# Optimization experiments

Measured on AMD Instinct MI355X. Metric: run time of the kernel, lower is better.

## Reference

```python
import jax, jax.numpy as jnp
import numpy as np


def _conv2d(x, w, pad):
    return jax.lax.conv_general_dilated(
        x, w, (1, 1), [(pad, pad), (pad, pad)],
        dimension_numbers=('NCHW', 'OIHW', 'NCHW'))


def _affine_grid(theta, k):
    # torch F.affine_grid, align_corners=False; output size (k, k)
    base = ((2.0 * jnp.arange(k) + 1.0) / k - 1.0).astype(jnp.float32)
    pts = jnp.stack([
        jnp.broadcast_to(base[None, :], (k, k)),  # x varies along width
        jnp.broadcast_to(base[:, None], (k, k)),  # y varies along height
        jnp.ones((k, k), jnp.float32)], -1)        # [k,k,3]
    return jnp.einsum('ijc,nrc->nijr', pts, theta)  # [N,k,k,2] -> (x,y)


def _grid_sample(img, grid):
    # torch F.grid_sample: bilinear, zeros padding, align_corners=False
    # img [C,H,W], grid [k,k,2] with (x,y) in [-1,1]
    C, H, W = img.shape
    gx = (grid[..., 0] + 1.0) * W * 0.5 - 0.5
    gy = (grid[..., 1] + 1.0) * H * 0.5 - 0.5
    x0 = jnp.floor(gx); y0 = jnp.floor(gy)
    wx = gx - x0; wy = gy - y0
    x0i = x0.astype(jnp.int32); y0i = y0.astype(jnp.int32)

    def gath(yi, xi):
        valid = ((xi >= 0) & (xi < W) & (yi >= 0) & (yi < H)).astype(img.dtype)
        v = img[:, jnp.clip(yi, 0, H - 1), jnp.clip(xi, 0, W - 1)]  # [C,k,k]
        return v * valid[None]

    v00 = gath(y0i, x0i); v01 = gath(y0i, x0i + 1)
    v10 = gath(y0i + 1, x0i); v11 = gath(y0i + 1, x0i + 1)
    return (v00 * ((1 - wx) * (1 - wy))[None] + v01 * (wx * (1 - wy))[None]
            + v10 * ((1 - wx) * wy)[None] + v11 * (wx * wy)[None])


def reference(x, stn0_w, stn0_b, stn1_w, lin_w, lin_b, check):
    B, C, H, W = x.shape
    k = stn1_w.shape[-1]
    h = jax.nn.relu(_conv2d(x, stn0_w, k // 2) + stn0_b[None, :, None, None])
    ident6 = jnp.array([1., 0., 0., 0., 1., 0.], jnp.float32)
    out = _conv2d(h, stn1_w, 0) * (1.0 - check) + ident6[None, :, None, None]
    Ho, Wo = out.shape[2], out.shape[3]
    N = B * Ho * Wo
    # permute(0,3,2,1).view(N,2,3) as in torch
    theta = out.transpose(0, 3, 2, 1).reshape(N, 2, 3)
    grid = _affine_grid(theta, k)  # [N,k,k,2]
    xv = jnp.arange(k // 2, k // 2 + Ho, dtype=jnp.float32)[:, None]  # meshgrid 'ij'
    yv = jnp.arange(k // 2, k // 2 + Wo, dtype=jnp.float32)[None, :]
    half = float(k // 2)
    auxx = ((grid[..., 0] * half).reshape(B, Ho, Wo, k, k)
            + xv[None, :, :, None, None]).reshape(N, k, k) / (H - 1) * 2.0 - 1.0
    auxy = ((grid[..., 1] * half).reshape(B, Ho, Wo, k, k)
            + yv[None, :, :, None, None]).reshape(N, k, k) / (W - 1) * 2.0 - 1.0
    auxgrid = jnp.stack([auxx, auxy], -1).reshape(B, Ho * Wo, k, k, 2)
    # tile(x,0,Ho*Wo) duplicates x[b] for each of its Ho*Wo grids; gather directly
    xs = jax.vmap(lambda img, g: jax.vmap(lambda gg: _grid_sample(img, gg))(g))(x, auxgrid)  # [B,P,C,k,k]
    x_out = xs.reshape(N, -1) @ lin_w.T + lin_b  # [N,O]
    score = x_out.reshape(B, Ho, Wo, -1).transpose(0, 3, 2, 1)  # [B,O,Wo,Ho] as in torch
    ident23 = jnp.array([[1., 0., 0.], [0., 1., 0.]], jnp.float32)
    return score, ident23[None] - theta, out, auxx, auxy


def setup_inputs() -> dict:
    key = jax.random.key(0)
    ks = jax.random.split(key, 6)
    C, O, k = 128, 256, 3
    B, H, W = 8, 56, 56
    x = jax.random.normal(ks[0], (B, C, H, W), jnp.float32)
    stn0_w = jax.random.normal(ks[1], (C, C, k, k), jnp.float32) * (1.0 / np.sqrt(C * k * k))
    stn0_b = jax.random.normal(ks[2], (C,), jnp.float32) * 0.01
    # original zero-inits stn1; use small random so theta is non-trivial
    stn1_w = jax.random.normal(ks[3], (6, C, k, k), jnp.float32) * 0.01
    lin_w = jax.random.normal(ks[4], (O, C * k * k), jnp.float32) * (1.0 / np.sqrt(C * k * k))
    lin_b = jax.random.normal(ks[5], (O,), jnp.float32) * 0.01
    return {'x': x, 'stn0_w': stn0_w, 'stn0_b': stn0_b, 'stn1_w': stn1_w,
            'lin_w': lin_w, 'lin_b': lin_b, 'check': 0}
```

## Files before the change

kernel.cpp:

```cpp
#include <hip/hip_runtime.h>

typedef __attribute__((ext_vector_type(4))) float f32x4;
typedef __attribute__((ext_vector_type(8))) short bf16x8;

#define OPLANE 2916
#define NN 23328
#define KDIM 1152
#define PLANE 3136
#define LDP 72

__device__ __forceinline__ unsigned short f2bf(float f) {
    unsigned u = __builtin_bit_cast(unsigned, f);
    u += 0x7fffu + ((u >> 16) & 1u);
    return (unsigned short)(u >> 16);
}
__device__ __forceinline__ float bf2f(unsigned short h) {
    unsigned u = ((unsigned)h) << 16;
    return __builtin_bit_cast(float, u);
}

__global__ __launch_bounds__(256) void k_prep(const float* __restrict__ w0,
                                              const float* __restrict__ lw,
                                              unsigned short* __restrict__ b1t,
                                              unsigned short* __restrict__ b2t) {
    int idx = blockIdx.x * 256 + threadIdx.x;
    if (idx < 147456) {
        int r = idx / KDIM, k = idx - r * KDIM;
        int ij = k >> 7, ic = k & 127;
        b1t[idx] = f2bf(w0[r * KDIM + ic * 9 + ij]);
    } else {
        int j = idx - 147456;
        int r = j / KDIM, k = j - r * KDIM;
        int ij = k >> 7, ic = k & 127;
        b2t[j] = f2bf(lw[r * KDIM + ic * 9 + ij]);
    }
}

__global__ __launch_bounds__(256) void k_nhwc(const float* __restrict__ x,
                                              unsigned short* __restrict__ xnh) {
    __shared__ unsigned short lds[56 * 132];
    const int y = blockIdx.x, b = blockIdx.y, tid = threadIdx.x;
    for (int i = tid; i < 7168; i += 256) {
        int ic = i / 56, xc = i - ic * 56;
        lds[xc * 132 + ic] = f2bf(x[(b * 128 + ic) * PLANE + y * 56 + xc]);
    }
    __syncthreads();
    for (int i = tid; i < 7168; i += 256) {
        int xc = i >> 7, ic = i & 127;
        xnh[(b * PLANE + y * 56 + xc) * 128 + ic] = lds[xc * 132 + ic];
    }
}

__global__ __launch_bounds__(256) void k_gemm1(const unsigned short* __restrict__ xnh,
                                               const unsigned short* __restrict__ Bt,
                                               const float* __restrict__ bias,
                                               float* __restrict__ C) {
    __shared__ unsigned short As[64 * LDP];
    __shared__ unsigned short Bs[64 * LDP];
    const int tid = threadIdx.x;
    const int lane = tid & 63, wid = tid >> 6;
    const int wr = wid >> 1, wc = wid & 1;
    const int n0 = blockIdx.x * 64;
    const int m0 = blockIdx.y * 64;

    f32x4 acc[2][2];
    #pragma unroll
    for (int mt = 0; mt < 2; mt++)
        #pragma unroll
        for (int nt = 0; nt < 2; nt++) { acc[mt][nt][0]=0.f; acc[mt][nt][1]=0.f; acc[mt][nt][2]=0.f; acc[mt][nt][3]=0.f; }

    const int row = tid >> 2, q = tid & 3;
    const int p = m0 + row;
    const int b = p / PLANE; int rem = p - b * PLANE;
    const int y = rem / 56; const int xc = rem - y * 56;
    unsigned short* asw = &As[row * LDP + q * 16];
    const unsigned short* bg = Bt + (n0 + row) * KDIM + q * 16;
    unsigned short* bsw = &Bs[row * LDP + q * 16];
    const int lm = lane & 15, lq = lane >> 4;

    uint4 a0, a1, bv0, bv1;
    auto issue = [&](int it) {
        const int ij = it >> 1;
        const int di = ij / 3, dj = ij - di * 3;
        const int icb = (it & 1) << 6;
        a0 = make_uint4(0u,0u,0u,0u); a1 = make_uint4(0u,0u,0u,0u);
        bool valid = (y + di >= 1) && (y + di <= 56) && (xc + dj >= 1) && (xc + dj <= 56);
        if (valid) {
            const unsigned short* ap = xnh + (p + (di - 1) * 56 + (dj - 1)) * 128 + icb + q * 16;
            a0 = *(const uint4*)ap;
            a1 = *(const uint4*)(ap + 8);
        }
        bv0 = *(const uint4*)(bg + it * 64);
        bv1 = *(const uint4*)(bg + it * 64 + 8);
    };
    issue(0);

    #pragma unroll
    for (int it = 0; it < 18; it++) {
        __syncthreads();
        *(uint4*)(asw + 0) = a0;  *(uint4*)(asw + 8) = a1;
        *(uint4*)(bsw + 0) = bv0; *(uint4*)(bsw + 8) = bv1;
        __syncthreads();
        if (it < 17) issue(it + 1);
        #pragma unroll
        for (int kk = 0; kk < 64; kk += 32) {
            bf16x8 af[2], bf[2];
            #pragma unroll
            for (int mt = 0; mt < 2; mt++)
                af[mt] = *(const bf16x8*)&As[(wr * 32 + mt * 16 + lm) * LDP + kk + lq * 8];
            #pragma unroll
            for (int nt = 0; nt < 2; nt++)
                bf[nt] = *(const bf16x8*)&Bs[(wc * 32 + nt * 16 + lm) * LDP + kk + lq * 8];
            #pragma unroll
            for (int mt = 0; mt < 2; mt++)
                #pragma unroll
                for (int nt = 0; nt < 2; nt++)
                    acc[mt][nt] = __builtin_amdgcn_mfma_f32_16x16x32_bf16(af[mt], bf[nt], acc[mt][nt], 0, 0, 0);
        }
    }
    #pragma unroll
    for (int mt = 0; mt < 2; mt++) {
        int m = m0 + wr * 32 + mt * 16 + lq * 4;
        #pragma unroll
        for (int nt = 0; nt < 2; nt++) {
            int n = n0 + wc * 32 + nt * 16 + lm;
            float bb = bias[n];
            #pragma unroll
            for (int r = 0; r < 4; r++)
                C[(m + r) * 128 + n] = fmaxf(acc[mt][nt][r] + bb, 0.f);
        }
    }
}

__global__ __launch_bounds__(256) void k_conv2f(const float* __restrict__ h,
                                                const float* __restrict__ w1,
                                                const int* __restrict__ check,
                                                float* __restrict__ o_out,
                                                float* __restrict__ o_th,
                                                float* __restrict__ o_ax,
                                                float* __restrict__ o_ay,
                                                float* __restrict__ sxy) {
    __shared__ float wlds[6912];
    __shared__ float red[16 * 6 * 17];
    __shared__ float vals[96];
    const int tid = threadIdx.x;
    for (int idx = tid; idx < 6912; idx += 256) {
        int r = idx / KDIM, k = idx - r * KDIM;
        int ij = k >> 7, ic = k & 127;
        wlds[idx] = w1[r * KDIM + ic * 9 + ij];
    }
    __syncthreads();
    const int pt = tid >> 4, c = tid & 15;
    const int p = blockIdx.x * 16 + pt;
    int b = p / OPLANE; int rem = p - b * OPLANE; int oh = rem / 54; int ow = rem - oh * 54;
    const float4* h4 = (const float4*)h;
    const float4* w4 = (const float4*)wlds;
    float acc[6] = {0.f, 0.f, 0.f, 0.f, 0.f, 0.f};
    const int base_sp = b * PLANE + oh * 56 + ow;
    #pragma unroll
    for (int i = 0; i < 3; i++) {
        #pragma unroll
        for (int j = 0; j < 3; j++) {
            int sp = base_sp + i * 56 + j;
            float4 h0 = h4[sp * 32 + c * 2];
            float4 h1 = h4[sp * 32 + c * 2 + 1];
            int ij = i * 3 + j;
            #pragma unroll
            for (int r = 0; r < 6; r++) {
                float4 wa = w4[r * 288 + ij * 32 + c * 2];
                float4 wb = w4[r * 288 + ij * 32 + c * 2 + 1];
                acc[r] += h0.x * wa.x + h0.y * wa.y + h0.z * wa.z + h0.w * wa.w
                        + h1.x * wb.x + h1.y * wb.y + h1.z * wb.z + h1.w * wb.w;
            }
        }
    }
    #pragma unroll
    for (int r = 0; r < 6; r++) red[(pt * 6 + r) * 17 + c] = acc[r];
    __syncthreads();
    if (tid < 96) {
        const float* rp = &red[tid * 17];
        float s = 0.f;
        #pragma unroll
        for (int e = 0; e < 16; e++) s += rp[e];
        vals[tid] = s;
    }
    __syncthreads();
    if (tid < 16) {
        int p2 = blockIdx.x * 16 + tid;
        int b2 = p2 / OPLANE; int r2 = p2 - b2 * OPLANE; int oh2 = r2 / 54; int ow2 = r2 - oh2 * 54;
        float val[6];
        float s = 1.0f - (float)check[0];
        const float id6[6] = {1.f, 0.f, 0.f, 0.f, 1.f, 0.f};
        #pragma unroll
        for (int r = 0; r < 6; r++) val[r] = vals[tid * 6 + r] * s + id6[r];
        int n = (b2 * 54 + ow2) * 54 + oh2;
        #pragma unroll
        for (int r = 0; r < 6; r++) {
            o_out[((b2 * 6 + r) * 54 + oh2) * 54 + ow2] = val[r];
            o_th[n * 6 + r] = id6[r] - val[r];
        }
        const float bse[3] = {-2.f / 3.f, 0.f, 2.f / 3.f};
        #pragma unroll
        for (int i = 0; i < 3; i++)
            #pragma unroll
            for (int j = 0; j < 3; j++) {
                float gx = bse[j] * val[0] + bse[i] * val[1] + val[2];
                float gy = bse[j] * val[3] + bse[i] * val[4] + val[5];
                float ax = (gx + 1.f + (float)ow2) * (2.f / 55.f) - 1.f;
                float ay = (gy + 1.f + (float)oh2) * (2.f / 55.f) - 1.f;
                int ij = i * 3 + j;
                o_ax[n * 9 + ij] = ax;
                o_ay[n * 9 + ij] = ay;
                sxy[(n * 9 + ij) * 2 + 0] = (ax + 1.f) * 28.f - 0.5f;
                sxy[(n * 9 + ij) * 2 + 1] = (ay + 1.f) * 28.f - 0.5f;
            }
    }
}

__global__ __launch_bounds__(256) void k_sgemm(const unsigned short* __restrict__ xnh,
                                               const unsigned short* __restrict__ Wt,
                                               const float* __restrict__ bias,
                                               const float* __restrict__ sxy,
                                               float* __restrict__ score) {
    __shared__ unsigned short Ss[64 * LDP];
    __shared__ unsigned short Ws[128 * LDP];
    const int tid = threadIdx.x;
    const int lane = tid & 63, wid = tid >> 6;
    const int wr = wid >> 1, wc = wid & 1;
    const int o0 = blockIdx.x * 128;
    const int s0 = blockIdx.y * 64;

    f32x4 acc[4][2];
    #pragma unroll
    for (int mt = 0; mt < 4; mt++)
        #pragma unroll
        for (int nt = 0; nt < 2; nt++) { acc[mt][nt][0]=0.f; acc[mt][nt][1]=0.f; acc[mt][nt][2]=0.f; acc[mt][nt][3]=0.f; }

    const int row = tid >> 2, q = tid & 3;
    const int mp = min(s0 + row, NN - 1);
    const int b = mp / OPLANE; const int rr = mp - b * OPLANE;
    const int ho = rr / 54, wo = rr - (rr / 54) * 54;
    const int n = (b * 54 + wo) * 54 + ho;
    const int xbase = b * PLANE;
    unsigned short* ssw = &Ss[row * LDP + q * 16];
    const int wrow = tid >> 1, wq = tid & 1;
    const unsigned short* wg = Wt + (o0 + wrow) * KDIM + wq * 32;
    unsigned short* wsw = &Ws[wrow * LDP + wq * 32];
    const int lm = lane & 15, lq = lane >> 4;

    float2 sc[9];
    {
        const float* spp = sxy + n * 18;
        #pragma unroll
        for (int ij = 0; ij < 9; ij++) sc[ij] = *(const float2*)(spp + ij * 2);
    }

    int off0 = 0, off1 = 0, off2 = 0, off3 = 0;
    float wt0 = 0.f, wt1 = 0.f, wt2 = 0.f, wt3 = 0.f;
    auto mkoff = [&](int ij) {
        float sx = sc[ij].x, sy = sc[ij].y;
        float x0f = floorf(sx), y0f = floorf(sy);
        float wx = sx - x0f, wy = sy - y0f;
        int x0 = (int)x0f, y0 = (int)y0f;
        int x1 = x0 + 1, y1 = y0 + 1;
        float vx0 = (x0 >= 0 && x0 < 56) ? 1.f : 0.f;
        float vx1 = (x1 >= 0 && x1 < 56) ? 1.f : 0.f;
        float vy0 = (y0 >= 0 && y0 < 56) ? 1.f : 0.f;
        float vy1 = (y1 >= 0 && y1 < 56) ? 1.f : 0.f;
        int xc0 = min(max(x0, 0), 55), xc1 = min(max(x1, 0), 55);
        int yc0 = min(max(y0, 0), 55), yc1 = min(max(y1, 0), 55);
        off0 = (xbase + yc0 * 56 + xc0) << 7;
        off1 = (xbase + yc0 * 56 + xc1) << 7;
        off2 = (xbase + yc1 * 56 + xc0) << 7;
        off3 = (xbase + yc1 * 56 + xc1) << 7;
        wt0 = vy0 * vx0 * (1.f - wx) * (1.f - wy);
        wt1 = vy0 * vx1 * wx * (1.f - wy);
        wt2 = vy1 * vx0 * (1.f - wx) * wy;
        wt3 = vy1 * vx1 * wx * wy;
    };

    uint4 p0a, p0b, p1a, p1b, p2a, p2b, p3a, p3b;
    uint4 w0v, w1v, w2v, w3v;
    auto issue = [&](int it) {
        const int co = ((it & 1) << 6) + q * 16;
        p0a = *(const uint4*)(xnh + off0 + co);
        p0b = *(const uint4*)(xnh + off0 + co + 8);
        p1a = *(const uint4*)(xnh + off1 + co);
        p1b = *(const uint4*)(xnh + off1 + co + 8);
        p2a = *(const uint4*)(xnh + off2 + co);
        p2b = *(const uint4*)(xnh + off2 + co + 8);
        p3a = *(const uint4*)(xnh + off3 + co);
        p3b = *(const uint4*)(xnh + off3 + co + 8);
        w0v = *(const uint4*)(wg + it * 64);
        w1v = *(const uint4*)(wg + it * 64 + 8);
        w2v = *(const uint4*)(wg + it * 64 + 16);
        w3v = *(const uint4*)(wg + it * 64 + 24);
    };

    mkoff(0);
    issue(0);

    #pragma unroll
    for (int it = 0; it < 18; it++) {
        unsigned dw[8];
        const unsigned* d0 = (const unsigned*)&p0a;
        const unsigned* d1 = (const unsigned*)&p1a;
        const unsigned* d2 = (const unsigned*)&p2a;
        const unsigned* d3 = (const unsigned*)&p3a;
        const unsigned* e0 = (const unsigned*)&p0b;
        const unsigned* e1 = (const unsigned*)&p1b;
        const unsigned* e2 = (const unsigned*)&p2b;
        const unsigned* e3 = (const unsigned*)&p3b;
        #pragma unroll
        for (int d = 0; d < 8; d++) {
            unsigned u0 = (d < 4) ? d0[d] : e0[d - 4];
            unsigned u1 = (d < 4) ? d1[d] : e1[d - 4];
            unsigned u2 = (d < 4) ? d2[d] : e2[d - 4];
            unsigned u3 = (d < 4) ? d3[d] : e3[d - 4];
            float lo = wt0 * __builtin_bit_cast(float, u0 << 16)
                     + wt1 * __builtin_bit_cast(float, u1 << 16)
                     + wt2 * __builtin_bit_cast(float, u2 << 16)
                     + wt3 * __builtin_bit_cast(float, u3 << 16);
            float hi = wt0 * __builtin_bit_cast(float, u0 & 0xffff0000u)
                     + wt1 * __builtin_bit_cast(float, u1 & 0xffff0000u)
                     + wt2 * __builtin_bit_cast(float, u2 & 0xffff0000u)
                     + wt3 * __builtin_bit_cast(float, u3 & 0xffff0000u);
            dw[d] = (unsigned)f2bf(lo) | ((unsigned)f2bf(hi) << 16);
        }
        __syncthreads();
        *(uint4*)(ssw + 0) = *(uint4*)&dw[0];
        *(uint4*)(ssw + 8) = *(uint4*)&dw[4];
        *(uint4*)(wsw + 0)  = w0v;
        *(uint4*)(wsw + 8)  = w1v;
        *(uint4*)(wsw + 16) = w2v;
        *(uint4*)(wsw + 24) = w3v;
        __syncthreads();
        if (it < 17) {
            if (((it + 1) & 1) == 0) mkoff((it + 1) >> 1);
            issue(it + 1);
        }
        #pragma unroll
        for (int kk = 0; kk < 64; kk += 32) {
            bf16x8 wf[4], sf[2];
            #pragma unroll
            for (int mt = 0; mt < 4; mt++)
                wf[mt] = *(const bf16x8*)&Ws[(wr * 64 + mt * 16 + lm) * LDP + kk + lq * 8];
            #pragma unroll
            for (int nt = 0; nt < 2; nt++)
                sf[nt] = *(const bf16x8*)&Ss[(wc * 32 + nt * 16 + lm) * LDP + kk + lq * 8];
            #pragma unroll
            for (int mt = 0; mt < 4; mt++)
                #pragma unroll
                for (int nt = 0; nt < 2; nt++)
                    acc[mt][nt] = __builtin_amdgcn_mfma_f32_16x16x32_bf16(wf[mt], sf[nt], acc[mt][nt], 0, 0, 0);
        }
    }
    #pragma unroll
    for (int mt = 0; mt < 4; mt++) {
        #pragma unroll
        for (int r = 0; r < 4; r++) {
            int o = o0 + wr * 64 + mt * 16 + lq * 4 + r;
            float bb = bias[o];
            #pragma unroll
            for (int nt = 0; nt < 2; nt++) {
                int s = s0 + wc * 32 + nt * 16 + lm;
                if (s < NN) {
                    int sb = s / OPLANE;
                    int soff = s - sb * OPLANE;
                    score[(sb * 256 + o) * OPLANE + soff] = acc[mt][nt][r] + bb;
                }
            }
        }
    }
}

extern "C" void kernel_launch(void* const* d_in, const int* in_sizes, int n_in,
                              void* d_out, int out_size, void* d_ws, size_t ws_size,
                              hipStream_t stream) {
    const float* x  = (const float*)d_in[0];
    const float* w0 = (const float*)d_in[1];
    const float* b0 = (const float*)d_in[2];
    const float* w1 = (const float*)d_in[3];
    const float* lw = (const float*)d_in[4];
    const float* lb = (const float*)d_in[5];
    const int* check = (const int*)d_in[6];

    float* out   = (float*)d_out;
    float* score = out;
    float* o_th  = out + 5971968;
    float* o_out = out + 6111936;
    float* o_ax  = out + 6251904;
    float* o_ay  = out + 6461856;

    char* wsb = (char*)d_ws;
    float* h   = (float*)wsb;
    unsigned short* xnh = (unsigned short*)(wsb + 12845056);
    unsigned short* b1t = (unsigned short*)(wsb + 19267584);
    unsigned short* b2t = (unsigned short*)(wsb + 19562496);
    float* sxy = (float*)(wsb + 20152320);

    k_prep<<<1728, 256, 0, stream>>>(w0, lw, b1t, b2t);
    k_nhwc<<<dim3(56, 8), 256, 0, stream>>>(x, xnh);
    k_gemm1<<<dim3(2, 392), 256, 0, stream>>>(xnh, b1t, b0, h);
    k_conv2f<<<1458, 256, 0, stream>>>(h, w1, check, o_out, o_th, o_ax, o_ay, sxy);
    k_sgemm<<<dim3(2, 365), 256, 0, stream>>>(xnh, b2t, lb, sxy, score);
}
```

Before: 168.9 us.

## Double K-tile in conv GEMM and pack bilinear blend math

```diff
diff --git a/kernel.cpp b/kernel.cpp
--- a/kernel.cpp
+++ b/kernel.cpp
@@ -1,6 +1,7 @@
 #include <hip/hip_runtime.h>
 
 typedef __attribute__((ext_vector_type(4))) float f32x4;
+typedef __attribute__((ext_vector_type(2))) float f32x2;
 typedef __attribute__((ext_vector_type(8))) short bf16x8;
 
 #define OPLANE 2916
@@ -8,15 +9,16 @@
 #define KDIM 1152
 #define PLANE 3136
 #define LDP 72
+#define LDP2 136
 
 __device__ __forceinline__ unsigned short f2bf(float f) {
     unsigned u = __builtin_bit_cast(unsigned, f);
     u += 0x7fffu + ((u >> 16) & 1u);
     return (unsigned short)(u >> 16);
 }
-__device__ __forceinline__ float bf2f(unsigned short h) {
-    unsigned u = ((unsigned)h) << 16;
-    return __builtin_bit_cast(float, u);
+
+__device__ __forceinline__ void keep(const uint4& v) {
+    asm volatile("" :: "v"(v.x), "v"(v.y), "v"(v.z), "v"(v.w));
 }
 
 __global__ __launch_bounds__(256) void k_prep(const float* __restrict__ w0,
@@ -55,8 +57,8 @@
                                                const unsigned short* __restrict__ Bt,
                                                const float* __restrict__ bias,
                                                float* __restrict__ C) {
-    __shared__ unsigned short As[64 * LDP];
-    __shared__ unsigned short Bs[64 * LDP];
+    __shared__ unsigned short As[64 * LDP2];
+    __shared__ unsigned short Bs[64 * LDP2];
     const int tid = threadIdx.x;
     const int lane = tid & 63, wid = tid >> 6;
     const int wr = wid >> 1, wc = wid & 1;
@@ -73,44 +75,52 @@
     const int p = m0 + row;
     const int b = p / PLANE; int rem = p - b * PLANE;
     const int y = rem / 56; const int xc = rem - y * 56;
-    unsigned short* asw = &As[row * LDP + q * 16];
-    const unsigned short* bg = Bt + (n0 + row) * KDIM + q * 16;
-    unsigned short* bsw = &Bs[row * LDP + q * 16];
+    unsigned short* asw = &As[row * LDP2 + q * 32];
+    const unsigned short* bg = Bt + (n0 + row) * KDIM + q * 32;
+    unsigned short* bsw = &Bs[row * LDP2 + q * 32];
     const int lm = lane & 15, lq = lane >> 4;
 
-    uint4 a0, a1, bv0, bv1;
-    auto issue = [&](int it) {
-        const int ij = it >> 1;
+    uint4 a0, a1, a2, a3, b0, b1, b2, b3;
+    auto issue = [&](int ij) {
         const int di = ij / 3, dj = ij - di * 3;
-        const int icb = (it & 1) << 6;
-        a0 = make_uint4(0u,0u,0u,0u); a1 = make_uint4(0u,0u,0u,0u);
+        a0 = make_uint4(0u,0u,0u,0u); a1 = a0; a2 = a0; a3 = a0;
         bool valid = (y + di >= 1) && (y + di <= 56) && (xc + dj >= 1) && (xc + dj <= 56);
+        const unsigned short* bp = bg + ij * 128;
+        b0 = *(const uint4*)(bp + 0);
+        b1 = *(const uint4*)(bp + 8);
+        b2 = *(const uint4*)(bp + 16);
+        b3 = *(const uint4*)(bp + 24);
         if (valid) {
-            const unsigned short* ap = xnh + (p + (di - 1) * 56 + (dj - 1)) * 128 + icb + q * 16;
-            a0 = *(const uint4*)ap;
+            const unsigned short* ap = xnh + (p + (di - 1) * 56 + (dj - 1)) * 128 + q * 32;
+            a0 = *(const uint4*)(ap + 0);
             a1 = *(const uint4*)(ap + 8);
-        }
-        bv0 = *(const uint4*)(bg + it * 64);
-        bv1 = *(const uint4*)(bg + it * 64 + 8);
+            a2 = *(const uint4*)(ap + 16);
+            a3 = *(const uint4*)(ap + 24);
+        }
     };
     issue(0);
 
     #pragma unroll
-    for (int it = 0; it < 18; it++) {
+    for (int it = 0; it < 9; it++) {
+        keep(a0); keep(a1); keep(a2); keep(a3);
+        keep(b0); keep(b1); keep(b2); keep(b3);
         __syncthreads();
-        *(uint4*)(asw + 0) = a0;  *(uint4*)(asw + 8) = a1;
-        *(uint4*)(bsw + 0) = bv0; *(uint4*)(bsw + 8) = bv1;
+        *(uint4*)(asw + 0)  = a0; *(uint4*)(asw + 8)  = a1;
+        *(uint4*)(asw + 16) = a2; *(uint4*)(asw + 24) = a3;
+        *(uint4*)(bsw + 0)  = b0; *(uint4*)(bsw + 8)  = b1;
+        *(uint4*)(bsw + 16) = b2; *(uint4*)(bsw + 24) = b3;
         __syncthreads();
-        if (it < 17) issue(it + 1);
-        #pragma unroll
-        for (int kk = 0; kk < 64; kk += 32) {
+        if (it < 8) issue(it + 1);
+        __builtin_amdgcn_sched_barrier(0);
+        #pragma unroll
+        for (int kk = 0; kk < 128; kk += 32) {
             bf16x8 af[2], bf[2];
             #pragma unroll
             for (int mt = 0; mt < 2; mt++)
-                af[mt] = *(const bf16x8*)&As[(wr * 32 + mt * 16 + lm) * LDP + kk + lq * 8];
+                af[mt] = *(const bf16x8*)&As[(wr * 32 + mt * 16 + lm) * LDP2 + kk + lq * 8];
             #pragma unroll
             for (int nt = 0; nt < 2; nt++)
-                bf[nt] = *(const bf16x8*)&Bs[(wc * 32 + nt * 16 + lm) * LDP + kk + lq * 8];
+                bf[nt] = *(const bf16x8*)&Bs[(wc * 32 + nt * 16 + lm) * LDP2 + kk + lq * 8];
             #pragma unroll
             for (int mt = 0; mt < 2; mt++)
                 #pragma unroll
@@ -256,7 +266,7 @@
     }
 
     int off0 = 0, off1 = 0, off2 = 0, off3 = 0;
-    float wt0 = 0.f, wt1 = 0.f, wt2 = 0.f, wt3 = 0.f;
+    f32x2 W0, W1, W2, W3;
     auto mkoff = [&](int ij) {
         float sx = sc[ij].x, sy = sc[ij].y;
         float x0f = floorf(sx), y0f = floorf(sy);
@@ -273,15 +283,23 @@
         off1 = (xbase + yc0 * 56 + xc1) << 7;
         off2 = (xbase + yc1 * 56 + xc0) << 7;
         off3 = (xbase + yc1 * 56 + xc1) << 7;
-        wt0 = vy0 * vx0 * (1.f - wx) * (1.f - wy);
-        wt1 = vy0 * vx1 * wx * (1.f - wy);
-        wt2 = vy1 * vx0 * (1.f - wx) * wy;
-        wt3 = vy1 * vx1 * wx * wy;
+        float wt0 = vy0 * vx0 * (1.f - wx) * (1.f - wy);
+        float wt1 = vy0 * vx1 * wx * (1.f - wy);
+        float wt2 = vy1 * vx0 * (1.f - wx) * wy;
+        float wt3 = vy1 * vx1 * wx * wy;
+        W0[0] = wt0; W0[1] = wt0;
+        W1[0] = wt1; W1[1] = wt1;
+        W2[0] = wt2; W2[1] = wt2;
+        W3[0] = wt3; W3[1] = wt3;
     };
 
     uint4 p0a, p0b, p1a, p1b, p2a, p2b, p3a, p3b;
     uint4 w0v, w1v, w2v, w3v;
     auto issue = [&](int it) {
+        w0v = *(const uint4*)(wg + it * 64);
+        w1v = *(const uint4*)(wg + it * 64 + 8);
+        w2v = *(const uint4*)(wg + it * 64 + 16);
+        w3v = *(const uint4*)(wg + it * 64 + 24);
         const int co = ((it & 1) << 6) + q * 16;
         p0a = *(const uint4*)(xnh + off0 + co);
         p0b = *(const uint4*)(xnh + off0 + co + 8);
@@ -291,10 +309,6 @@
         p2b = *(const uint4*)(xnh + off2 + co + 8);
         p3a = *(const uint4*)(xnh + off3 + co);
         p3b = *(const uint4*)(xnh + off3 + co + 8);
-        w0v = *(const uint4*)(wg + it * 64);
-        w1v = *(const uint4*)(wg + it * 64 + 8);
-        w2v = *(const uint4*)(wg + it * 64 + 16);
-        w3v = *(const uint4*)(wg + it * 64 + 24);
     };
 
     mkoff(0);
@@ -317,15 +331,22 @@
             unsigned u1 = (d < 4) ? d1[d] : e1[d - 4];
             unsigned u2 = (d < 4) ? d2[d] : e2[d - 4];
             unsigned u3 = (d < 4) ? d3[d] : e3[d - 4];
-            float lo = wt0 * __builtin_bit_cast(float, u0 << 16)
-                     + wt1 * __builtin_bit_cast(float, u1 << 16)
-                     + wt2 * __builtin_bit_cast(float, u2 << 16)
-                     + wt3 * __builtin_bit_cast(float, u3 << 16);
-            float hi = wt0 * __builtin_bit_cast(float, u0 & 0xffff0000u)
-                     + wt1 * __builtin_bit_cast(float, u1 & 0xffff0000u)
-                     + wt2 * __builtin_bit_cast(float, u2 & 0xffff0000u)
-                     + wt3 * __builtin_bit_cast(float, u3 & 0xffff0000u);
-            dw[d] = (unsigned)f2bf(lo) | ((unsigned)f2bf(hi) << 16);
+            f32x2 v, a2;
+            v[0] = __builtin_bit_cast(float, u0 << 16);
+            v[1] = __builtin_bit_cast(float, u0 & 0xffff0000u);
+            asm("v_pk_mul_f32 %0, %1, %2" : "=v"(a2) : "v"(W0), "v"(v));
+            v[0] = __builtin_bit_cast(float, u1 << 16);
+            v[1] = __builtin_bit_cast(float, u1 & 0xffff0000u);
+            asm("v_pk_fma_f32 %0, %1, %2, %0" : "+v"(a2) : "v"(W1), "v"(v));
+            v[0] = __builtin_bit_cast(float, u2 << 16);
+            v[1] = __builtin_bit_cast(float, u2 & 0xffff0000u);
+            asm("v_pk_fma_f32 %0, %1, %2, %0" : "+v"(a2) : "v"(W2), "v"(v));
+            v[0] = __builtin_bit_cast(float, u3 << 16);
+            v[1] = __builtin_bit_cast(float, u3 & 0xffff0000u);
+            asm("v_pk_fma_f32 %0, %1, %2, %0" : "+v"(a2) : "v"(W3), "v"(v));
+            unsigned pk;
+            asm("v_cvt_pk_bf16_f32 %0, %1, %2" : "=v"(pk) : "v"(a2[0]), "v"(a2[1]));
+            dw[d] = pk;
         }
         __syncthreads();
         *(uint4*)(ssw + 0) = *(uint4*)&dw[0];
@@ -339,6 +360,7 @@
             if (((it + 1) & 1) == 0) mkoff((it + 1) >> 1);
             issue(it + 1);
         }
+        __builtin_amdgcn_sched_barrier(0);
         #pragma unroll
         for (int kk = 0; kk < 64; kk += 32) {
             bf16x8 wf[4], sf[2];
```

Measured after the change: 182.7 us. +8.1%, slower.

## Restructure sampling GEMM: full-O blocks, direct weight fragments, double-buffered samples

Applied to the files above, without the earlier changes.

```diff
diff --git a/kernel.cpp b/kernel.cpp
--- a/kernel.cpp
+++ b/kernel.cpp
@@ -13,10 +13,6 @@
     unsigned u = __builtin_bit_cast(unsigned, f);
     u += 0x7fffu + ((u >> 16) & 1u);
     return (unsigned short)(u >> 16);
-}
-__device__ __forceinline__ float bf2f(unsigned short h) {
-    unsigned u = ((unsigned)h) << 16;
-    return __builtin_bit_cast(float, u);
 }
 
 __global__ __launch_bounds__(256) void k_prep(const float* __restrict__ w0,
@@ -222,13 +218,10 @@
                                                const float* __restrict__ bias,
                                                const float* __restrict__ sxy,
                                                float* __restrict__ score) {
-    __shared__ unsigned short Ss[64 * LDP];
-    __shared__ unsigned short Ws[128 * LDP];
+    __shared__ unsigned short Ss[2][32 * LDP];
     const int tid = threadIdx.x;
     const int lane = tid & 63, wid = tid >> 6;
-    const int wr = wid >> 1, wc = wid & 1;
-    const int o0 = blockIdx.x * 128;
-    const int s0 = blockIdx.y * 64;
+    const int s0 = blockIdx.x * 32;
 
     f32x4 acc[4][2];
     #pragma unroll
@@ -236,17 +229,16 @@
         #pragma unroll
         for (int nt = 0; nt < 2; nt++) { acc[mt][nt][0]=0.f; acc[mt][nt][1]=0.f; acc[mt][nt][2]=0.f; acc[mt][nt][3]=0.f; }
 
-    const int row = tid >> 2, q = tid & 3;
-    const int mp = min(s0 + row, NN - 1);
+    const int row = tid >> 3, q = tid & 7;
+    const int mp = s0 + row;
     const int b = mp / OPLANE; const int rr = mp - b * OPLANE;
     const int ho = rr / 54, wo = rr - (rr / 54) * 54;
     const int n = (b * 54 + wo) * 54 + ho;
     const int xbase = b * PLANE;
-    unsigned short* ssw = &Ss[row * LDP + q * 16];
-    const int wrow = tid >> 1, wq = tid & 1;
-    const unsigned short* wg = Wt + (o0 + wrow) * KDIM + wq * 32;
-    unsigned short* wsw = &Ws[wrow * LDP + wq * 32];
+    unsigned short* ssw0 = &Ss[0][row * LDP + q * 8];
+    unsigned short* ssw1 = &Ss[1][row * LDP + q * 8];
     const int lm = lane & 15, lq = lane >> 4;
+    const unsigned short* wgb = Wt + (wid * 64 + lm) * KDIM + lq * 8;
 
     float2 sc[9];
     {
@@ -279,44 +271,23 @@
         wt3 = vy1 * vx1 * wx * wy;
     };
 
-    uint4 p0a, p0b, p1a, p1b, p2a, p2b, p3a, p3b;
-    uint4 w0v, w1v, w2v, w3v;
+    uint4 p0, p1, p2, p3;
     auto issue = [&](int it) {
-        const int co = ((it & 1) << 6) + q * 16;
-        p0a = *(const uint4*)(xnh + off0 + co);
-        p0b = *(const uint4*)(xnh + off0 + co + 8);
-        p1a = *(const uint4*)(xnh + off1 + co);
-        p1b = *(const uint4*)(xnh + off1 + co + 8);
-        p2a = *(const uint4*)(xnh + off2 + co);
-        p2b = *(const uint4*)(xnh + off2 + co + 8);
-        p3a = *(const uint4*)(xnh + off3 + co);
-        p3b = *(const uint4*)(xnh + off3 + co + 8);
-        w0v = *(const uint4*)(wg + it * 64);
-        w1v = *(const uint4*)(wg + it * 64 + 8);
-        w2v = *(const uint4*)(wg + it * 64 + 16);
-        w3v = *(const uint4*)(wg + it * 64 + 24);
+        const int co = ((it & 1) << 6) + q * 8;
+        p0 = *(const uint4*)(xnh + off0 + co);
+        p1 = *(const uint4*)(xnh + off1 + co);
+        p2 = *(const uint4*)(xnh + off2 + co);
+        p3 = *(const uint4*)(xnh + off3 + co);
     };
-
-    mkoff(0);
-    issue(0);
-
-    #pragma unroll
-    for (int it = 0; it < 18; it++) {
-        unsigned dw[8];
-        const unsigned* d0 = (const unsigned*)&p0a;
-        const unsigned* d1 = (const unsigned*)&p1a;
-        const unsigned* d2 = (const unsigned*)&p2a;
-        const unsigned* d3 = (const unsigned*)&p3a;
-        const unsigned* e0 = (const unsigned*)&p0b;
-        const unsigned* e1 = (const unsigned*)&p1b;
-        const unsigned* e2 = (const unsigned*)&p2b;
-        const unsigned* e3 = (const unsigned*)&p3b;
-        #pragma unroll
-        for (int d = 0; d < 8; d++) {
-            unsigned u0 = (d < 4) ? d0[d] : e0[d - 4];
-            unsigned u1 = (d < 4) ? d1[d] : e1[d - 4];
-            unsigned u2 = (d < 4) ? d2[d] : e2[d - 4];
-            unsigned u3 = (d < 4) ? d3[d] : e3[d - 4];
+    auto blendv = [&]() -> uint4 {
+        unsigned dwv[4];
+        const unsigned* c0 = (const unsigned*)&p0;
+        const unsigned* c1 = (const unsigned*)&p1;
+        const unsigned* c2 = (const unsigned*)&p2;
+        const unsigned* c3 = (const unsigned*)&p3;
+        #pragma unroll
+        for (int d = 0; d < 4; d++) {
+            unsigned u0 = c0[d], u1 = c1[d], u2 = c2[d], u3 = c3[d];
             float lo = wt0 * __builtin_bit_cast(float, u0 << 16)
                      + wt1 * __builtin_bit_cast(float, u1 << 16)
                      + wt2 * __builtin_bit_cast(float, u2 << 16)
@@ -325,18 +296,21 @@
                      + wt1 * __builtin_bit_cast(float, u1 & 0xffff0000u)
                      + wt2 * __builtin_bit_cast(float, u2 & 0xffff0000u)
                      + wt3 * __builtin_bit_cast(float, u3 & 0xffff0000u);
-            dw[d] = (unsigned)f2bf(lo) | ((unsigned)f2bf(hi) << 16);
-        }
-        __syncthreads();
-        *(uint4*)(ssw + 0) = *(uint4*)&dw[0];
-        *(uint4*)(ssw + 8) = *(uint4*)&dw[4];
-        *(uint4*)(wsw + 0)  = w0v;
-        *(uint4*)(wsw + 8)  = w1v;
-        *(uint4*)(wsw + 16) = w2v;
-        *(uint4*)(wsw + 24) = w3v;
-        __syncthreads();
+            dwv[d] = (unsigned)f2bf(lo) | ((unsigned)f2bf(hi) << 16);
+        }
+        return *(uint4*)dwv;
+    };
+
+    mkoff(0);
+    issue(0);
+    *(uint4*)ssw0 = blendv();
+    __syncthreads();
+
+    #pragma unroll
+    for (int it = 0; it < 18; it++) {
+        const int cur = it & 1;
         if (it < 17) {
-            if (((it + 1) & 1) == 0) mkoff((it + 1) >> 1);
+            if ((((it + 1) & 1)) == 0) mkoff((it + 1) >> 1);
             issue(it + 1);
         }
         #pragma unroll
@@ -344,31 +318,33 @@
             bf16x8 wf[4], sf[2];
             #pragma unroll
             for (int mt = 0; mt < 4; mt++)
-                wf[mt] = *(const bf16x8*)&Ws[(wr * 64 + mt * 16 + lm) * LDP + kk + lq * 8];
+                wf[mt] = *(const bf16x8*)(wgb + mt * 16 * KDIM + it * 64 + kk);
             #pragma unroll
             for (int nt = 0; nt < 2; nt++)
-                sf[nt] = *(const bf16x8*)&Ss[(wc * 32 + nt * 16 + lm) * LDP + kk + lq * 8];
+                sf[nt] = *(const bf16x8*)&Ss[cur][(nt * 16 + lm) * LDP + kk + lq * 8];
             #pragma unroll
             for (int mt = 0; mt < 4; mt++)
                 #pragma unroll
                 for (int nt = 0; nt < 2; nt++)
                     acc[mt][nt] = __builtin_amdgcn_mfma_f32_16x16x32_bf16(wf[mt], sf[nt], acc[mt][nt], 0, 0, 0);
         }
+        if (it < 17) {
+            *(uint4*)(cur ? ssw0 : ssw1) = blendv();
+            __syncthreads();
+        }
     }
     #pragma unroll
     for (int mt = 0; mt < 4; mt++) {
         #pragma unroll
         for (int r = 0; r < 4; r++) {
-            int o = o0 + wr * 64 + mt * 16 + lq * 4 + r;
+            int o = wid * 64 + mt * 16 + lq * 4 + r;
             float bb = bias[o];
             #pragma unroll
             for (int nt = 0; nt < 2; nt++) {
-                int s = s0 + wc * 32 + nt * 16 + lm;
-                if (s < NN) {
-                    int sb = s / OPLANE;
-                    int soff = s - sb * OPLANE;
-                    score[(sb * 256 + o) * OPLANE + soff] = acc[mt][nt][r] + bb;
-                }
+                int s = s0 + nt * 16 + lm;
+                int sb = s / OPLANE;
+                int soff = s - sb * OPLANE;
+                score[(sb * 256 + o) * OPLANE + soff] = acc[mt][nt][r] + bb;
             }
         }
     }
@@ -403,5 +379,5 @@
     k_nhwc<<<dim3(56, 8), 256, 0, stream>>>(x, xnh);
     k_gemm1<<<dim3(2, 392), 256, 0, stream>>>(xnh, b1t, b0, h);
     k_conv2f<<<1458, 256, 0, stream>>>(h, w1, check, o_out, o_th, o_ax, o_ay, sxy);
-    k_sgemm<<<dim3(2, 365), 256, 0, stream>>>(xnh, b2t, lb, sxy, score);
-}
+    k_sgemm<<<729, 256, 0, stream>>>(xnh, b2t, lb, sxy, score);
+}
```

New measurement: 185.7 us. 1.1x slower.

## Merge prep kernels and widen conv GEMM block to cover all 128 outputs

Applied to the files above, without the earlier changes.

```diff
diff --git a/kernel.cpp b/kernel.cpp
--- a/kernel.cpp
+++ b/kernel.cpp
@@ -14,54 +14,51 @@
     u += 0x7fffu + ((u >> 16) & 1u);
     return (unsigned short)(u >> 16);
 }
-__device__ __forceinline__ float bf2f(unsigned short h) {
-    unsigned u = ((unsigned)h) << 16;
-    return __builtin_bit_cast(float, u);
-}
-
-__global__ __launch_bounds__(256) void k_prep(const float* __restrict__ w0,
-                                              const float* __restrict__ lw,
-                                              unsigned short* __restrict__ b1t,
-                                              unsigned short* __restrict__ b2t) {
-    int idx = blockIdx.x * 256 + threadIdx.x;
-    if (idx < 147456) {
-        int r = idx / KDIM, k = idx - r * KDIM;
-        int ij = k >> 7, ic = k & 127;
-        b1t[idx] = f2bf(w0[r * KDIM + ic * 9 + ij]);
+
+__global__ __launch_bounds__(256) void k_pre(const float* __restrict__ x,
+                                             const float* __restrict__ w0,
+                                             const float* __restrict__ lw,
+                                             unsigned short* __restrict__ xnh,
+                                             unsigned short* __restrict__ b1t,
+                                             unsigned short* __restrict__ b2t) {
+    __shared__ unsigned short lds[56 * 132];
+    if (blockIdx.x < 1728) {
+        int idx = blockIdx.x * 256 + threadIdx.x;
+        if (idx < 147456) {
+            int r = idx / KDIM, k = idx - r * KDIM;
+            int ij = k >> 7, ic = k & 127;
+            b1t[idx] = f2bf(w0[r * KDIM + ic * 9 + ij]);
+        } else {
+            int j = idx - 147456;
+            int r = j / KDIM, k = j - r * KDIM;
+            int ij = k >> 7, ic = k & 127;
+            b2t[j] = f2bf(lw[r * KDIM + ic * 9 + ij]);
+        }
     } else {
-        int j = idx - 147456;
-        int r = j / KDIM, k = j - r * KDIM;
-        int ij = k >> 7, ic = k & 127;
-        b2t[j] = f2bf(lw[r * KDIM + ic * 9 + ij]);
-    }
-}
-
-__global__ __launch_bounds__(256) void k_nhwc(const float* __restrict__ x,
-                                              unsigned short* __restrict__ xnh) {
-    __shared__ unsigned short lds[56 * 132];
-    const int y = blockIdx.x, b = blockIdx.y, tid = threadIdx.x;
-    for (int i = tid; i < 7168; i += 256) {
-        int ic = i / 56, xc = i - ic * 56;
-        lds[xc * 132 + ic] = f2bf(x[(b * 128 + ic) * PLANE + y * 56 + xc]);
-    }
-    __syncthreads();
-    for (int i = tid; i < 7168; i += 256) {
-        int xc = i >> 7, ic = i & 127;
-        xnh[(b * PLANE + y * 56 + xc) * 128 + ic] = lds[xc * 132 + ic];
-    }
-}
-
-__global__ __launch_bounds__(256) void k_gemm1(const unsigned short* __restrict__ xnh,
+        const int bid = blockIdx.x - 1728;
+        const int y = bid % 56, b = bid / 56, tid = threadIdx.x;
+        for (int i = tid; i < 7168; i += 256) {
+            int ic = i / 56, xc = i - ic * 56;
+            lds[xc * 132 + ic] = f2bf(x[(b * 128 + ic) * PLANE + y * 56 + xc]);
+        }
+        __syncthreads();
+        for (int i = tid; i < 7168; i += 256) {
+            int xc = i >> 7, ic = i & 127;
+            xnh[(b * PLANE + y * 56 + xc) * 128 + ic] = lds[xc * 132 + ic];
+        }
+    }
+}
+
+__global__ __launch_bounds__(512) void k_gemm1(const unsigned short* __restrict__ xnh,
                                                const unsigned short* __restrict__ Bt,
                                                const float* __restrict__ bias,
                                                float* __restrict__ C) {
     __shared__ unsigned short As[64 * LDP];
-    __shared__ unsigned short Bs[64 * LDP];
+    __shared__ unsigned short Bs[128 * LDP];
     const int tid = threadIdx.x;
     const int lane = tid & 63, wid = tid >> 6;
-    const int wr = wid >> 1, wc = wid & 1;
-    const int n0 = blockIdx.x * 64;
-    const int m0 = blockIdx.y * 64;
+    const int wr = wid >> 2, wc = wid & 3;
+    const int m0 = blockIdx.x * 64;
 
     f32x4 acc[2][2];
     #pragma unroll
@@ -69,26 +66,26 @@
         #pragma unroll
         for (int nt = 0; nt < 2; nt++) { acc[mt][nt][0]=0.f; acc[mt][nt][1]=0.f; acc[mt][nt][2]=0.f; acc[mt][nt][3]=0.f; }
 
-    const int row = tid >> 2, q = tid & 3;
+    const int row = tid >> 3, q = tid & 7;
     const int p = m0 + row;
     const int b = p / PLANE; int rem = p - b * PLANE;
     const int y = rem / 56; const int xc = rem - y * 56;
-    unsigned short* asw = &As[row * LDP + q * 16];
-    const unsigned short* bg = Bt + (n0 + row) * KDIM + q * 16;
-    unsigned short* bsw = &Bs[row * LDP + q * 16];
+    unsigned short* asw = &As[row * LDP + q * 8];
+    const int brow = tid >> 2, bq = tid & 3;
+    const unsigned short* bg = Bt + brow * KDIM + bq * 16;
+    unsigned short* bsw = &Bs[brow * LDP + bq * 16];
     const int lm = lane & 15, lq = lane >> 4;
 
-    uint4 a0, a1, bv0, bv1;
+    uint4 a0, bv0, bv1;
     auto issue = [&](int it) {
         const int ij = it >> 1;
         const int di = ij / 3, dj = ij - di * 3;
         const int icb = (it & 1) << 6;
-        a0 = make_uint4(0u,0u,0u,0u); a1 = make_uint4(0u,0u,0u,0u);
+        a0 = make_uint4(0u,0u,0u,0u);
         bool valid = (y + di >= 1) && (y + di <= 56) && (xc + dj >= 1) && (xc + dj <= 56);
         if (valid) {
-            const unsigned short* ap = xnh + (p + (di - 1) * 56 + (dj - 1)) * 128 + icb + q * 16;
+            const unsigned short* ap = xnh + (p + (di - 1) * 56 + (dj - 1)) * 128 + icb + q * 8;
             a0 = *(const uint4*)ap;
-            a1 = *(const uint4*)(ap + 8);
         }
         bv0 = *(const uint4*)(bg + it * 64);
         bv1 = *(const uint4*)(bg + it * 64 + 8);
@@ -98,7 +95,7 @@
     #pragma unroll
     for (int it = 0; it < 18; it++) {
         __syncthreads();
-        *(uint4*)(asw + 0) = a0;  *(uint4*)(asw + 8) = a1;
+        *(uint4*)asw = a0;
         *(uint4*)(bsw + 0) = bv0; *(uint4*)(bsw + 8) = bv1;
         __syncthreads();
         if (it < 17) issue(it + 1);
@@ -123,7 +120,7 @@
         int m = m0 + wr * 32 + mt * 16 + lq * 4;
         #pragma unroll
         for (int nt = 0; nt < 2; nt++) {
-            int n = n0 + wc * 32 + nt * 16 + lm;
+            int n = wc * 32 + nt * 16 + lm;
             float bb = bias[n];
             #pragma unroll
             for (int r = 0; r < 4; r++)
@@ -399,9 +396,8 @@
     unsigned short* b2t = (unsigned short*)(wsb + 19562496);
     float* sxy = (float*)(wsb + 20152320);
 
-    k_prep<<<1728, 256, 0, stream>>>(w0, lw, b1t, b2t);
-    k_nhwc<<<dim3(56, 8), 256, 0, stream>>>(x, xnh);
-    k_gemm1<<<dim3(2, 392), 256, 0, stream>>>(xnh, b1t, b0, h);
+    k_pre<<<2176, 256, 0, stream>>>(x, w0, lw, xnh, b1t, b2t);
+    k_gemm1<<<392, 512, 0, stream>>>(xnh, b1t, b0, h);
     k_conv2f<<<1458, 256, 0, stream>>>(h, w1, check, o_out, o_th, o_ax, o_ay, sxy);
     k_sgemm<<<dim3(2, 365), 256, 0, stream>>>(xnh, b2t, lb, sxy, score);
 }
```

Measured after the change: 167.0 us. Within noise of the previous version (-1.1%).
